# Kernel optimization log

Hardware: AMD Instinct MI355X
Metric: run time of the kernel (lower is better)

The kernel has to match this reference:

```python
import jax, jax.numpy as jnp
import numpy as np
from jax import lax

B = 64          # batch
IMG = 384       # image H=W
PATCH = 16      # stem patch size -> 24x24 grid
C = 192         # hidden_channels
K = 5           # knn_graph k (hard-coded in extract_graph)
HG = IMG // PATCH
N = HG * HG     # total_num_nodes = 576
HID = 4 * C     # FFN expansion
PRED_HID = 1024
NUM_CLASSES = 1


def setup_inputs() -> dict:
    key = jax.random.key(0)
    ks = jax.random.split(key, 16)
    def w(k, shape, s=0.02):
        return jax.random.normal(k, shape, jnp.float32) * s
    f32 = jnp.float32
    return {
        "x": jax.random.normal(ks[0], (B, 3, IMG, IMG), f32),
        # stem: 16x16 patch-embed conv
        "stem_w": w(ks[1], (C, 3, PATCH, PATCH)),
        "stem_b": jnp.zeros((C,), f32),
        "pos_embed": w(ks[2], (1, C, HG, HG)),
        # GSAT edge-attention MLP: concat(src,dst) -> C -> 1 -> sigmoid
        "att_w1": w(ks[3], (2 * C, C)), "att_b1": jnp.zeros((C,), f32),
        "att_w2": w(ks[4], (C, 1)),     "att_b2": jnp.zeros((1,), f32),
        # two message-passing layers (GIN-style update)
        "gnn_w1": w(ks[5], (C, C)), "gnn_b1": jnp.zeros((C,), f32),
        "gnn_w2": w(ks[6], (C, C)), "gnn_b2": jnp.zeros((C,), f32),
        # FFN (1x1 convs == channel matmuls), BN in eval mode (mean0/var1)
        "ffn_w1": w(ks[7], (C, HID)), "ffn_b1": jnp.zeros((HID,), f32),
        "ffn_g1": jnp.ones((HID,), f32), "ffn_be1": jnp.zeros((HID,), f32),
        "ffn_w2": w(ks[8], (HID, C)), "ffn_b2": jnp.zeros((C,), f32),
        "ffn_g2": jnp.ones((C,), f32), "ffn_be2": jnp.zeros((C,), f32),
        # prediction head: 1x1 conv C->1024, BN(eval), gelu, 1x1 conv 1024->num_classes
        "pred_w1": w(ks[9], (C, PRED_HID)), "pred_b1": jnp.zeros((PRED_HID,), f32),
        "pred_g": jnp.ones((PRED_HID,), f32), "pred_be": jnp.zeros((PRED_HID,), f32),
        "pred_w2": w(ks[10], (PRED_HID, NUM_CLASSES)), "pred_b2": jnp.zeros((NUM_CLASSES,), f32),
    }


def reference(x, stem_w, stem_b, pos_embed,
              att_w1, att_b1, att_w2, att_b2,
              gnn_w1, gnn_b1, gnn_w2, gnn_b2,
              ffn_w1, ffn_b1, ffn_g1, ffn_be1,
              ffn_w2, ffn_b2, ffn_g2, ffn_be2,
              pred_w1, pred_b1, pred_g, pred_be, pred_w2, pred_b2):
    # ---- stem + pos_embed ----
    feat = lax.conv_general_dilated(x, stem_w, (PATCH, PATCH), 'VALID',
                                    dimension_numbers=('NCHW', 'OIHW', 'NCHW'))
    feat = feat + stem_b[None, :, None, None] + pos_embed        # [B,C,Hg,Wg]
    b, c, hg, wg = feat.shape
    n = hg * wg
    nf = feat.reshape(b, c, n).transpose(0, 2, 1)                # [B,N,C]
    nfd = lax.stop_gradient(nf)                                  # extract_graph under no_grad

    # ---- kNN graph build: per-image pairwise sq. distances + top-k ----
    sq = jnp.sum(nfd * nfd, axis=-1)                             # [B,N]
    d2 = sq[:, :, None] + sq[:, None, :] - 2.0 * jnp.einsum('bnc,bmc->bnm', nfd, nfd)
    d2 = d2 + jnp.eye(n, dtype=d2.dtype) * 1e9                   # exclude self-loops
    _, idx = lax.top_k(-d2, K)                                   # [B,N,K] nearest neighbors
    src = (idx + (jnp.arange(b) * n)[:, None, None]).reshape(-1)  # [E] global neighbor idx
    dst = jnp.repeat(jnp.arange(b * n), K)                        # [E] global center idx

    # ---- GSAT GNN: edge attention + attention-weighted message passing ----
    h = nfd.reshape(b * n, c)                                    # [BN,C] (detached)
    e = jax.nn.relu(jnp.concatenate([h[src], h[dst]], axis=-1) @ att_w1 + att_b1)
    edge_att = jax.nn.sigmoid(e @ att_w2 + att_b2)               # [E,1]
    for Wg, bg in ((gnn_w1, gnn_b1), (gnn_w2, gnn_b2)):
        m = jax.ops.segment_sum(edge_att * h[src], dst, num_segments=b * n)
        h = jax.nn.relu((h + m) @ Wg + bg)                       # GIN-style update

    # ---- FFN (1x1 convs) with residual, BN eval-mode affine ----
    t = h.reshape(b, n, c)                                       # [B,N,C]
    u = jax.nn.gelu((t @ ffn_w1 + ffn_b1) * ffn_g1 + ffn_be1, approximate=False)
    t = t + ((u @ ffn_w2 + ffn_b2) * ffn_g2 + ffn_be2)

    # ---- global average pool + prediction head ----
    g = jnp.mean(t, axis=1)                                      # [B,C]
    p = jax.nn.gelu((g @ pred_w1 + pred_b1) * pred_g + pred_be, approximate=False)
    prediction = p @ pred_w2 + pred_b2                           # [B,num_classes]
    return edge_att, prediction
```

## Files before the change

### kernel.cpp

```cpp
#include <hip/hip_runtime.h>
#include <hip/hip_bf16.h>
#include <math.h>

constexpr int B_    = 64;
constexpr int C_    = 192;
constexpr int N_    = 576;
constexpr int BN_   = B_ * N_;
constexpr int K_    = 5;
constexpr int E_    = BN_ * K_;

__device__ __forceinline__ float gelu_exact(float x) {
    return 0.5f * x * (1.0f + erff(x * 0.70710678118654752440f));
}

__device__ __forceinline__ float bf2f(unsigned short v) {
    return __uint_as_float(((unsigned)v) << 16);
}
__device__ __forceinline__ unsigned short f2bf(float x) {
    __hip_bfloat16 h = __float2bfloat16(x);
    return *(unsigned short*)&h;
}

__global__ __launch_bounds__(256) void transpose_w_k(const float* __restrict__ w,
                                                     float* __restrict__ wt) {
    int gid = blockIdx.x * 256 + threadIdx.x;
    int k = gid / 192, oc = gid % 192;
    wt[gid] = w[oc * 768 + k];
}

__global__ __launch_bounds__(256) void stem_gemm96_k(
    const float* __restrict__ x, const float* __restrict__ Wt,
    const float* __restrict__ sb, const float* __restrict__ pos,
    float* __restrict__ nf)
{
    __shared__ float As[96][68];
    __shared__ float Ws[64][68];
    const int tid = threadIdx.x;
    const int tr = tid >> 4, tc = tid & 15;
    const int mb = blockIdx.x;
    const int nb = blockIdx.y;
    const int b  = mb / 6;
    const int n0 = (mb % 6) * 96;

    float4 acc[6];
    #pragma unroll
    for (int i = 0; i < 6; ++i) acc[i] = float4{0.f, 0.f, 0.f, 0.f};

    for (int kc = 0; kc < 768; kc += 64) {
        #pragma unroll
        for (int i = 0; i < 6; ++i) {
            int q = i * 256 + tid;
            int m = q >> 4, kq = q & 15;
            int k = kc + kq * 4;
            int ci = k >> 8, rem = k & 255, dy = rem >> 4, dx = rem & 15;
            int n = n0 + m, py = n / 24, px = n % 24;
            const float* src = &x[(((size_t)(b * 3 + ci) * 384) + py * 16 + dy) * 384
                                  + px * 16 + dx];
            *(float4*)&As[m][kq * 4] = *(const float4*)src;
        }
        #pragma unroll
        for (int i = 0; i < 4; ++i) {
            int q = i * 256 + tid;
            int m = q >> 4, kq = q & 15;
            *(float4*)&Ws[m][kq * 4] =
                *(const float4*)&Wt[(size_t)(kc + m) * 192 + nb * 64 + kq * 4];
        }
        __syncthreads();
        #pragma unroll
        for (int k4 = 0; k4 < 64; k4 += 4) {
            float4 a4[6], b4[4];
            #pragma unroll
            for (int i = 0; i < 6; ++i) a4[i] = *(const float4*)&As[tr * 6 + i][k4];
            #pragma unroll
            for (int kk = 0; kk < 4; ++kk) b4[kk] = *(const float4*)&Ws[k4 + kk][tc * 4];
            #pragma unroll
            for (int i = 0; i < 6; ++i) {
                const float av[4] = {a4[i].x, a4[i].y, a4[i].z, a4[i].w};
                #pragma unroll
                for (int kk = 0; kk < 4; ++kk) {
                    acc[i].x += av[kk] * b4[kk].x;
                    acc[i].y += av[kk] * b4[kk].y;
                    acc[i].z += av[kk] * b4[kk].z;
                    acc[i].w += av[kk] * b4[kk].w;
                }
            }
        }
        __syncthreads();
    }

    #pragma unroll
    for (int i = 0; i < 6; ++i) {
        int n = n0 + tr * 6 + i;
        int row = b * 576 + n;
        int oc0 = nb * 64 + tc * 4;
        float v[4] = {acc[i].x, acc[i].y, acc[i].z, acc[i].w};
        #pragma unroll
        for (int j = 0; j < 4; ++j) {
            int oc = oc0 + j;
            v[j] = v[j] + sb[oc] + pos[oc * 576 + n];
        }
        *(float4*)&nf[(size_t)row * 192 + oc0] = float4{v[0], v[1], v[2], v[3]};
    }
}

__global__ __launch_bounds__(256) void sq_k(const float* __restrict__ nf,
                                            float* __restrict__ sq) {
    int wid = threadIdx.x >> 6, lane = threadIdx.x & 63;
    int n = blockIdx.x * 4 + wid;
    const float* row = nf + (size_t)n * 192;
    float s = 0.f;
    #pragma unroll
    for (int c = 0; c < 3; ++c) { float v = row[lane + c * 64]; s += v * v; }
    #pragma unroll
    for (int off = 32; off; off >>= 1) s += __shfl_down(s, off);
    if (lane == 0) sq[n] = s;
}

__global__ void transpose_nf_k(const float* __restrict__ nf, float* __restrict__ nfT) {
    __shared__ float tile[32][33];
    int b = blockIdx.z;
    int n0 = blockIdx.x * 32, c0 = blockIdx.y * 32;
    int tx = threadIdx.x, ty = threadIdx.y;
    #pragma unroll
    for (int r = 0; r < 4; ++r) {
        int i = ty * 4 + r;
        tile[i][tx] = nf[((size_t)b * 576 + n0 + i) * 192 + c0 + tx];
    }
    __syncthreads();
    #pragma unroll
    for (int r = 0; r < 4; ++r) {
        int i = ty * 4 + r;
        nfT[((size_t)b * 192 + c0 + i) * 576 + n0 + tx] = tile[tx][i];
    }
}

__global__ __launch_bounds__(256) void knn_part_k(
    const float* __restrict__ nf, const float* __restrict__ nfT,
    const float* __restrict__ sqn, float* __restrict__ candV,
    int* __restrict__ candI)
{
    __shared__ float As[64][68];
    __shared__ float Cs[64][68];
    __shared__ float d2s[64][69];
    const int tid = threadIdx.x;
    const int tr = tid >> 4, tc = tid & 15;
    const int b = blockIdx.x;
    const int row0 = blockIdx.y * 64;
    const int gz = blockIdx.z;
    const int cc0 = gz * 3;

    float* mergeV = (float*)&As[0][0];
    int*   mergeI = (int*)&Cs[0][0];

    float tv[5];
    int ti[5];
    #pragma unroll
    for (int p = 0; p < 5; ++p) { tv[p] = 3.4e38f; ti[p] = 0; }

    for (int cc = cc0; cc < cc0 + 3; ++cc) {
        float4 acc[4];
        acc[0] = acc[1] = acc[2] = acc[3] = float4{0.f, 0.f, 0.f, 0.f};
        for (int kc = 0; kc < 192; kc += 64) {
            #pragma unroll
            for (int i = 0; i < 4; ++i) {
                int q = i * 256 + tid;
                int m = q >> 4, kq = q & 15;
                *(float4*)&As[m][kq * 4] =
                    *(const float4*)&nf[((size_t)(b * 576 + row0 + m)) * 192 + kc + kq * 4];
                *(float4*)&Cs[m][kq * 4] =
                    *(const float4*)&nfT[((size_t)(b * 192 + kc + m)) * 576 + cc * 64 + kq * 4];
            }
            __syncthreads();
            #pragma unroll
            for (int k4 = 0; k4 < 64; k4 += 4) {
                float4 a4[4], b4[4];
                #pragma unroll
                for (int i = 0; i < 4; ++i) a4[i] = *(const float4*)&As[tr * 4 + i][k4];
                #pragma unroll
                for (int kk = 0; kk < 4; ++kk) b4[kk] = *(const float4*)&Cs[k4 + kk][tc * 4];
                #pragma unroll
                for (int i = 0; i < 4; ++i) {
                    const float av[4] = {a4[i].x, a4[i].y, a4[i].z, a4[i].w};
                    #pragma unroll
                    for (int kk = 0; kk < 4; ++kk) {
                        acc[i].x += av[kk] * b4[kk].x;
                        acc[i].y += av[kk] * b4[kk].y;
                        acc[i].z += av[kk] * b4[kk].z;
                        acc[i].w += av[kk] * b4[kk].w;
                    }
                }
            }
            __syncthreads();
        }
        #pragma unroll
        for (int i = 0; i < 4; ++i) {
            int rl = tr * 4 + i, rg = row0 + rl;
            float sr = sqn[b * 576 + rg];
            float vv[4] = {acc[i].x, acc[i].y, acc[i].z, acc[i].w};
            #pragma unroll
            for (int j = 0; j < 4; ++j) {
                int cl = tc * 4 + j, cg = cc * 64 + cl;
                float d = sr + sqn[b * 576 + cg] - 2.f * vv[j];
                if (cg == rg) d += 1e9f;
                d2s[rl][cl] = d;
            }
        }
        __syncthreads();

        {
            const int r = tid & 63, p = tid >> 6;
            float pv[5]; int pi[5];
            #pragma unroll
            for (int q = 0; q < 5; ++q) { pv[q] = 3.4e38f; pi[q] = 0x7fffffff; }
            #pragma unroll
            for (int j = 0; j < 16; ++j) {
                int c = p * 16 + j;
                float cv = d2s[r][c];
                if (cv < pv[4]) {
                    int ci = cc * 64 + c;
                    #pragma unroll
                    for (int q = 0; q < 5; ++q) {
                        bool less = cv < pv[q];
                        float nv = less ? pv[q] : cv;
                        int ni   = less ? pi[q] : ci;
                        pv[q] = less ? cv : pv[q];
                        pi[q] = less ? ci : pi[q];
                        cv = nv; ci = ni;
                    }
                }
            }
            #pragma unroll
            for (int q = 0; q < 5; ++q) {
                mergeV[r * 21 + p * 5 + q] = pv[q];
                mergeI[r * 21 + p * 5 + q] = pi[q];
            }
        }
        __syncthreads();
        if (tid < 64) {
            for (int s = 0; s < 20; ++s) {
                float cv = mergeV[tid * 21 + s];
                if (cv < tv[4]) {
                    int cidx = mergeI[tid * 21 + s];
                    #pragma unroll
                    for (int q = 0; q < 5; ++q) {
                        bool less = cv < tv[q];
                        float nv = less ? tv[q] : cv;
                        int ni   = less ? ti[q] : cidx;
                        tv[q] = less ? cv : tv[q];
                        ti[q] = less ? cidx : ti[q];
                        cv = nv; cidx = ni;
                    }
                }
            }
        }
        __syncthreads();
    }
    if (tid < 64) {
        int gr = b * 576 + row0 + tid;
        #pragma unroll
        for (int p = 0; p < 5; ++p) {
            candV[(size_t)gr * 15 + gz * 5 + p] = tv[p];
            candI[(size_t)gr * 15 + gz * 5 + p] = ti[p];
        }
    }
}

__global__ __launch_bounds__(256) void knn_merge_k(
    const float* __restrict__ candV, const int* __restrict__ candI,
    int* __restrict__ idxOut)
{
    int r = blockIdx.x * 256 + threadIdx.x;
    float tv[5]; int ti[5];
    #pragma unroll
    for (int p = 0; p < 5; ++p) { tv[p] = 3.4e38f; ti[p] = 0; }
    #pragma unroll
    for (int s = 0; s < 15; ++s) {
        float cv = candV[(size_t)r * 15 + s];
        if (cv < tv[4]) {
            int cidx = candI[(size_t)r * 15 + s];
            #pragma unroll
            for (int q = 0; q < 5; ++q) {
                bool less = cv < tv[q];
                float nv = less ? tv[q] : cv;
                int ni   = less ? ti[q] : cidx;
                tv[q] = less ? cv : tv[q];
                ti[q] = less ? cidx : ti[q];
                cv = nv; cidx = ni;
            }
        }
    }
    int base = (r / 576) * 576;
    #pragma unroll
    for (int p = 0; p < 5; ++p) idxOut[r * 5 + p] = base + ti[p];
}

template <int EPI>
__global__ __launch_bounds__(256) void gemm_rm_k(
    const float* __restrict__ A, const float* __restrict__ W, float* __restrict__ out,
    int M, int N, int K,
    const float* __restrict__ bias, const float* __restrict__ gsc,
    const float* __restrict__ gsh, const float* __restrict__ res)
{
    __shared__ float As[64][68];
    __shared__ float Ws[64][68];
    const int tid = threadIdx.x;
    const int tr = tid >> 4, tc = tid & 15;
    const int mBase = blockIdx.x * 64, nBase = blockIdx.y * 64;

    float4 acc[4];
    acc[0] = acc[1] = acc[2] = acc[3] = float4{0.f, 0.f, 0.f, 0.f};

    for (int kc = 0; kc < K; kc += 64) {
        #pragma unroll
        for (int i = 0; i < 4; ++i) {
            int q = i * 256 + tid;
            int m = q >> 4, kq = q & 15;
            *(float4*)&As[m][kq * 4] =
                *(const float4*)&A[(size_t)(mBase + m) * K + kc + kq * 4];
            *(float4*)&Ws[m][kq * 4] =
                *(const float4*)&W[(size_t)(kc + m) * N + nBase + kq * 4];
        }
        __syncthreads();
        #pragma unroll
        for (int k4 = 0; k4 < 64; k4 += 4) {
            float4 a4[4], b4[4];
            #pragma unroll
            for (int i = 0; i < 4; ++i) a4[i] = *(const float4*)&As[tr * 4 + i][k4];
            #pragma unroll
            for (int kk = 0; kk < 4; ++kk) b4[kk] = *(const float4*)&Ws[k4 + kk][tc * 4];
            #pragma unroll
            for (int i = 0; i < 4; ++i) {
                const float av[4] = {a4[i].x, a4[i].y, a4[i].z, a4[i].w};
                #pragma unroll
                for (int kk = 0; kk < 4; ++kk) {
                    acc[i].x += av[kk] * b4[kk].x;
                    acc[i].y += av[kk] * b4[kk].y;
                    acc[i].z += av[kk] * b4[kk].z;
                    acc[i].w += av[kk] * b4[kk].w;
                }
            }
        }
        __syncthreads();
    }

    #pragma unroll
    for (int i = 0; i < 4; ++i) {
        int row = mBase + tr * 4 + i;
        int n0 = nBase + tc * 4;
        float v[4] = {acc[i].x, acc[i].y, acc[i].z, acc[i].w};
        #pragma unroll
        for (int j = 0; j < 4; ++j) {
            int n = n0 + j;
            float xv = v[j];
            if (EPI == 1) xv += bias[n];
            if (EPI == 2) { xv += bias[n]; xv = fmaxf(xv, 0.f); }
            if (EPI == 3) { xv = (xv + bias[n]) * gsc[n] + gsh[n]; xv = gelu_exact(xv); }
            if (EPI == 4) {
                xv = res[(size_t)row * N + n] + (xv + bias[n]) * gsc[n] + gsh[n];
            }
            v[j] = xv;
        }
        *(float4*)&out[(size_t)row * N + n0] = float4{v[0], v[1], v[2], v[3]};
    }
}

template <int EPI>
__global__ __launch_bounds__(256) void gemm_mfma_k(
    const unsigned short* __restrict__ A, const unsigned short* __restrict__ Bt,
    unsigned short* __restrict__ out, int M, int N, int K,
    const float* __restrict__ bias, const float* __restrict__ gsc,
    const float* __restrict__ gsh, const unsigned short* __restrict__ res)
{
    using frag = __attribute__((ext_vector_type(8))) short;
    using facc = __attribute__((ext_vector_type(4))) float;
    __shared__ unsigned short As[64][72];
    __shared__ unsigned short Bs[64][72];
    const int tid = threadIdx.x;
    const int wave = tid >> 6, lane = tid & 63;
    const int m16 = lane & 15, quad = lane >> 4;
    const int mBase = blockIdx.x * 64, nBase = blockIdx.y * 64;

    facc zero = {0.f, 0.f, 0.f, 0.f};
    facc acc[4];
    #pragma unroll
    for (int t = 0; t < 4; ++t) acc[t] = zero;

    for (int kc = 0; kc < K; kc += 64) {
        #pragma unroll
        for (int r = 0; r < 2; ++r) {
            int q = r * 256 + tid;
            int row = q >> 3, c8 = (q & 7) * 8;
            *(int4*)&As[row][c8] =
                *(const int4*)&A[(size_t)(mBase + row) * K + kc + c8];
            *(int4*)&Bs[row][c8] =
                *(const int4*)&Bt[(size_t)(nBase + row) * K + kc + c8];
        }
        __syncthreads();
        #pragma unroll
        for (int kk = 0; kk < 64; kk += 32) {
            frag a = *(const frag*)&As[16 * wave + m16][kk + quad * 8];
            #pragma unroll
            for (int t = 0; t < 4; ++t) {
                frag b = *(const frag*)&Bs[t * 16 + m16][kk + quad * 8];
                acc[t] = __builtin_amdgcn_mfma_f32_16x16x32_bf16(a, b, acc[t], 0, 0, 0);
            }
        }
        __syncthreads();
    }

    #pragma unroll
    for (int t = 0; t < 4; ++t) {
        #pragma unroll
        for (int r = 0; r < 4; ++r) {
            int row = mBase + 16 * wave + quad * 4 + r;
            int col = nBase + t * 16 + m16;
            float xv = acc[t][r];
            if (EPI == 2) { xv += bias[col]; xv = fmaxf(xv, 0.f); }
            if (EPI == 3) { xv = (xv + bias[col]) * gsc[col] + gsh[col]; xv = gelu_exact(xv); }
            if (EPI == 4) {
                xv = bf2f(res[(size_t)row * N + col]) + (xv + bias[col]) * gsc[col] + gsh[col];
            }
            out[(size_t)row * N + col] = f2bf(xv);
        }
    }
}

template <int EPI>
__global__ __launch_bounds__(256) void gemm_mfma_split_k(
    const unsigned short* __restrict__ Ah, const unsigned short* __restrict__ Al,
    const unsigned short* __restrict__ Bh, const unsigned short* __restrict__ Bl,
    float* __restrict__ out, int M, int N, int K, const float* __restrict__ bias)
{
    using frag = __attribute__((ext_vector_type(8))) short;
    using facc = __attribute__((ext_vector_type(4))) float;
    __shared__ unsigned short AsH[64][72], AsL[64][72];
    __shared__ unsigned short BsH[64][72], BsL[64][72];
    const int tid = threadIdx.x;
    const int wave = tid >> 6, lane = tid & 63;
    const int m16 = lane & 15, quad = lane >> 4;
    const int mBase = blockIdx.x * 64, nBase = blockIdx.y * 64;

    facc zero = {0.f, 0.f, 0.f, 0.f};
    facc acc[4];
    #pragma unroll
    for (int t = 0; t < 4; ++t) acc[t] = zero;

    for (int kc = 0; kc < K; kc += 64) {
        #pragma unroll
        for (int r = 0; r < 2; ++r) {
            int q = r * 256 + tid;
            int row = q >> 3, c8 = (q & 7) * 8;
            *(int4*)&AsH[row][c8] = *(const int4*)&Ah[(size_t)(mBase + row) * K + kc + c8];
            *(int4*)&AsL[row][c8] = *(const int4*)&Al[(size_t)(mBase + row) * K + kc + c8];
            *(int4*)&BsH[row][c8] = *(const int4*)&Bh[(size_t)(nBase + row) * K + kc + c8];
            *(int4*)&BsL[row][c8] = *(const int4*)&Bl[(size_t)(nBase + row) * K + kc + c8];
        }
        __syncthreads();
        #pragma unroll
        for (int kk = 0; kk < 64; kk += 32) {
            frag ah = *(const frag*)&AsH[16 * wave + m16][kk + quad * 8];
            frag al = *(const frag*)&AsL[16 * wave + m16][kk + quad * 8];
            #pragma unroll
            for (int t = 0; t < 4; ++t) {
                frag bh = *(const frag*)&BsH[t * 16 + m16][kk + quad * 8];
                frag bl = *(const frag*)&BsL[t * 16 + m16][kk + quad * 8];
                acc[t] = __builtin_amdgcn_mfma_f32_16x16x32_bf16(ah, bh, acc[t], 0, 0, 0);
                acc[t] = __builtin_amdgcn_mfma_f32_16x16x32_bf16(ah, bl, acc[t], 0, 0, 0);
                acc[t] = __builtin_amdgcn_mfma_f32_16x16x32_bf16(al, bh, acc[t], 0, 0, 0);
            }
        }
        __syncthreads();
    }

    #pragma unroll
    for (int t = 0; t < 4; ++t) {
        #pragma unroll
        for (int r = 0; r < 4; ++r) {
            int row = mBase + 16 * wave + quad * 4 + r;
            int col = nBase + t * 16 + m16;
            float xv = acc[t][r];
            if (EPI == 1) xv += bias[col];
            out[(size_t)row * N + col] = xv;
        }
    }
}

__global__ __launch_bounds__(256) void asplit_k(const float* __restrict__ a,
                                                unsigned short* __restrict__ hi,
                                                unsigned short* __restrict__ lo) {
    int g = blockIdx.x * 256 + threadIdx.x;
    float v = a[g];
    unsigned short h = f2bf(v);
    hi[g] = h;
    lo[g] = f2bf(v - bf2f(h));
}

__global__ __launch_bounds__(256) void wsplit_att_k(const float* __restrict__ w,
                                                    unsigned short* __restrict__ hi,
                                                    unsigned short* __restrict__ lo) {
    int gid = blockIdx.x * 256 + threadIdx.x;
    int half = gid / 36864, r = gid % 36864;
    int n = r / 192, k = r % 192;
    float v = w[(size_t)(half * 192 + k) * 192 + n];
    unsigned short h = f2bf(v);
    hi[gid] = h;
    lo[gid] = f2bf(v - bf2f(h));
}

__global__ __launch_bounds__(256) void wprep_k(const float* __restrict__ w,
                                               unsigned short* __restrict__ wt,
                                               int K, int N) {
    int gid = blockIdx.x * 256 + threadIdx.x;
    int n = gid / K, k = gid % K;
    wt[gid] = f2bf(w[(size_t)k * N + n]);
}

__global__ __launch_bounds__(256) void edge_att_k(
    const float* __restrict__ hA, const float* __restrict__ hB,
    const int* __restrict__ idx, const float* __restrict__ w2,
    const float* __restrict__ b2, float* __restrict__ att)
{
    int wid = threadIdx.x >> 6, lane = threadIdx.x & 63;
    int e = blockIdx.x * 4 + wid;
    int dst = e / K_;
    int src = idx[e];
    float s = 0.f;
    #pragma unroll
    for (int c0 = 0; c0 < 3; ++c0) {
        int c = lane + c0 * 64;
        float v = hA[(size_t)src * 192 + c] + hB[(size_t)dst * 192 + c];
        v = fmaxf(v, 0.f);
        s += v * w2[c];
    }
    #pragma unroll
    for (int off = 32; off; off >>= 1) s += __shfl_down(s, off);
    if (lane == 0) att[e] = 1.f / (1.f + expf(-(s + b2[0])));
}

__device__ __forceinline__ float ldv(const float* p, size_t i) { return p[i]; }
__device__ __forceinline__ float ldv(const unsigned short* p, size_t i) { return bf2f(p[i]); }

template <typename TI>
__global__ __launch_bounds__(256) void msg_bf_k(
    const TI* __restrict__ h, const float* __restrict__ att,
    const int* __restrict__ idx, unsigned short* __restrict__ s)
{
    int g = blockIdx.x * 256 + threadIdx.x;
    int n = g / 192, c = g % 192;
    float acc = ldv(h, (size_t)g);
    #pragma unroll
    for (int p = 0; p < K_; ++p) {
        int sp = idx[n * K_ + p];
        acc += att[n * K_ + p] * ldv(h, (size_t)sp * 192 + c);
    }
    s[g] = f2bf(acc);
}

__global__ void pool_bf16_k(const unsigned short* __restrict__ t, float* __restrict__ g) {
    int b = blockIdx.x, c = threadIdx.x;
    float s = 0.f;
    for (int n = 0; n < 576; ++n) s += bf2f(t[((size_t)b * 576 + n) * 192 + c]);
    g[b * 192 + c] = s * (1.f / 576.f);
}

__global__ __launch_bounds__(256) void head2_k(
    const float* __restrict__ p, const float* __restrict__ w2,
    const float* __restrict__ b2, float* __restrict__ out)
{
    int b = blockIdx.x;
    float s = 0.f;
    for (int j = threadIdx.x; j < 1024; j += 256) s += p[(size_t)b * 1024 + j] * w2[j];
    #pragma unroll
    for (int off = 32; off; off >>= 1) s += __shfl_down(s, off);
    __shared__ float ls[4];
    int wid = threadIdx.x >> 6, lane = threadIdx.x & 63;
    if (lane == 0) ls[wid] = s;
    __syncthreads();
    if (threadIdx.x == 0) out[b] = ls[0] + ls[1] + ls[2] + ls[3] + b2[0];
}

extern "C" void kernel_launch(void* const* d_in, const int* in_sizes, int n_in,
                              void* d_out, int out_size, void* d_ws, size_t ws_size,
                              hipStream_t stream) {
    const float* x        = (const float*)d_in[0];
    const float* stem_w   = (const float*)d_in[1];
    const float* stem_b   = (const float*)d_in[2];
    const float* pos      = (const float*)d_in[3];
    const float* att_w1   = (const float*)d_in[4];
    const float* att_b1   = (const float*)d_in[5];
    const float* att_w2   = (const float*)d_in[6];
    const float* att_b2   = (const float*)d_in[7];
    const float* gnn_w1   = (const float*)d_in[8];
    const float* gnn_b1   = (const float*)d_in[9];
    const float* gnn_w2   = (const float*)d_in[10];
    const float* gnn_b2   = (const float*)d_in[11];
    const float* ffn_w1   = (const float*)d_in[12];
    const float* ffn_b1   = (const float*)d_in[13];
    const float* ffn_g1   = (const float*)d_in[14];
    const float* ffn_be1  = (const float*)d_in[15];
    const float* ffn_w2   = (const float*)d_in[16];
    const float* ffn_b2   = (const float*)d_in[17];
    const float* ffn_g2   = (const float*)d_in[18];
    const float* ffn_be2  = (const float*)d_in[19];
    const float* pred_w1  = (const float*)d_in[20];
    const float* pred_b1  = (const float*)d_in[21];
    const float* pred_g   = (const float*)d_in[22];
    const float* pred_be  = (const float*)d_in[23];
    const float* pred_w2  = (const float*)d_in[24];
    const float* pred_b2  = (const float*)d_in[25];

    float* ws = (float*)d_ws;
    const size_t RSZ = (size_t)BN_ * C_;
    float* R0 = ws;
    float* R1 = R0 + RSZ;
    float* R2 = R1 + RSZ;
    float* R3 = R2 + RSZ;
    float* sqb = R3 + RSZ;
    int*   idxb = (int*)(sqb + BN_);
    float* gb = (float*)(idxb + E_);
    float* pb = gb + 64 * C_;
    unsigned short* wg1T = (unsigned short*)(pb + 64 * 1024);
    unsigned short* wg2T = wg1T + 192 * 192;
    unsigned short* wf1T = wg2T + 192 * 192;
    unsigned short* wf2T = wf1T + 768 * 192;
    unsigned short* waHi = wf2T + 192 * 768;
    unsigned short* waLo = waHi + 2 * 192 * 192;
    float* candV = (float*)(waLo + 2 * 192 * 192);
    int*   candI = (int*)(candV + (size_t)BN_ * 15);

    unsigned short* Sb    = (unsigned short*)R1;
    unsigned short* Hb    = (unsigned short*)(R1 + RSZ / 2);
    unsigned short* Tb    = (unsigned short*)R2;
    unsigned short* ToutB = (unsigned short*)(R2 + RSZ / 2);
    unsigned short* Ahi   = (unsigned short*)R3;
    unsigned short* Alo   = Ahi + RSZ;
    unsigned short* Ub    = (unsigned short*)R3;

    float* att  = (float*)d_out;
    float* pred = att + E_;

    float* Wt = R3;

    wprep_k<<<144, 256, 0, stream>>>(gnn_w1, wg1T, 192, 192);
    wprep_k<<<144, 256, 0, stream>>>(gnn_w2, wg2T, 192, 192);
    wprep_k<<<576, 256, 0, stream>>>(ffn_w1, wf1T, 192, 768);
    wprep_k<<<576, 256, 0, stream>>>(ffn_w2, wf2T, 768, 192);
    wsplit_att_k<<<288, 256, 0, stream>>>(att_w1, waHi, waLo);

    transpose_w_k<<<576, 256, 0, stream>>>(stem_w, Wt);
    stem_gemm96_k<<<dim3(384, 3), 256, 0, stream>>>(x, Wt, stem_b, pos, R0);

    sq_k<<<BN_ / 4, 256, 0, stream>>>(R0, sqb);
    transpose_nf_k<<<dim3(18, 6, 64), dim3(32, 8), 0, stream>>>(R0, R3);
    knn_part_k<<<dim3(64, 9, 3), 256, 0, stream>>>(R0, R3, sqb, candV, candI);
    knn_merge_k<<<BN_ / 256, 256, 0, stream>>>(candV, candI, idxb);

    asplit_k<<<BN_ * C_ / 256, 256, 0, stream>>>(R0, Ahi, Alo);
    gemm_mfma_split_k<0><<<dim3(576, 3), 256, 0, stream>>>(Ahi, Alo,
        waHi, waLo, R1, BN_, 192, 192, nullptr);
    gemm_mfma_split_k<1><<<dim3(576, 3), 256, 0, stream>>>(Ahi, Alo,
        waHi + 36864, waLo + 36864, R2, BN_, 192, 192, att_b1);
    edge_att_k<<<E_ / 4, 256, 0, stream>>>(R1, R2, idxb, att_w2, att_b2, att);

    msg_bf_k<float><<<BN_ * C_ / 256, 256, 0, stream>>>(R0, att, idxb, Sb);
    gemm_mfma_k<2><<<dim3(576, 3), 256, 0, stream>>>(Sb, wg1T, Hb,
        BN_, 192, 192, gnn_b1, nullptr, nullptr, nullptr);
    msg_bf_k<unsigned short><<<BN_ * C_ / 256, 256, 0, stream>>>(Hb, att, idxb, Sb);
    gemm_mfma_k<2><<<dim3(576, 3), 256, 0, stream>>>(Sb, wg2T, Tb,
        BN_, 192, 192, gnn_b2, nullptr, nullptr, nullptr);

    for (int ch = 0; ch < 2; ++ch) {
        const unsigned short* Ain = Tb + (size_t)ch * 18432 * 192;
        unsigned short* Tout = ToutB + (size_t)ch * 18432 * 192;
        gemm_mfma_k<3><<<dim3(288, 12), 256, 0, stream>>>(Ain, wf1T, Ub,
            18432, 768, 192, ffn_b1, ffn_g1, ffn_be1, nullptr);
        gemm_mfma_k<4><<<dim3(288, 3), 256, 0, stream>>>(Ub, wf2T, Tout,
            18432, 192, 768, ffn_b2, ffn_g2, ffn_be2, Ain);
    }

    pool_bf16_k<<<64, 192, 0, stream>>>(ToutB, gb);
    gemm_rm_k<3><<<dim3(1, 16), 256, 0, stream>>>(gb, pred_w1, pb,
        64, 1024, 192, pred_b1, pred_g, pred_be, nullptr);
    head2_k<<<64, 256, 0, stream>>>(pb, pred_w2, pred_b2, pred);
}
```

Measured before the change: 808.2 us.

## Exploit distance symmetry in kNN: compute upper-triangle tiles once, emit both directions

Replaces the kNN partial kernel with one that computes only the 45 upper-triangular 64x64 tiles of each per-image distance matrix. Each tile produces top-5 candidates for its rows and, for off-diagonal tiles, also for its columns, so roughly half the distance GEMM work is removed. Blocks shrink to 64 threads with an 8x8 register tile, both operands are read from the transposed features, and candidate buffers are reused from an existing workspace region. The merge kernel now scans 45 candidates per row instead of 15. Smaller blocks and the serial 64-element scans per thread may lower occupancy and parallelism.

```diff
diff --git a/kernel.cpp b/kernel.cpp
--- a/kernel.cpp
+++ b/kernel.cpp
@@ -134,133 +134,124 @@
     }
 }
 
-__global__ __launch_bounds__(256) void knn_part_k(
-    const float* __restrict__ nf, const float* __restrict__ nfT,
-    const float* __restrict__ sqn, float* __restrict__ candV,
-    int* __restrict__ candI)
-{
-    __shared__ float As[64][68];
-    __shared__ float Cs[64][68];
-    __shared__ float d2s[64][69];
+__global__ __launch_bounds__(64) void knn_sym_k(
+    const float* __restrict__ nfT, const float* __restrict__ sqn,
+    float* __restrict__ candV, int* __restrict__ candI)
+{
+    __shared__ float smem[64 * 69];
+    float* As  = smem;
+    float* Bs  = smem + 2048;
+    float* d2s = smem;
+
     const int tid = threadIdx.x;
-    const int tr = tid >> 4, tc = tid & 15;
-    const int b = blockIdx.x;
-    const int row0 = blockIdx.y * 64;
-    const int gz = blockIdx.z;
-    const int cc0 = gz * 3;
-
-    float* mergeV = (float*)&As[0][0];
-    int*   mergeI = (int*)&Cs[0][0];
-
-    float tv[5];
-    int ti[5];
-    #pragma unroll
-    for (int p = 0; p < 5; ++p) { tv[p] = 3.4e38f; ti[p] = 0; }
-
-    for (int cc = cc0; cc < cc0 + 3; ++cc) {
-        float4 acc[4];
-        acc[0] = acc[1] = acc[2] = acc[3] = float4{0.f, 0.f, 0.f, 0.f};
-        for (int kc = 0; kc < 192; kc += 64) {
-            #pragma unroll
-            for (int i = 0; i < 4; ++i) {
-                int q = i * 256 + tid;
-                int m = q >> 4, kq = q & 15;
-                *(float4*)&As[m][kq * 4] =
-                    *(const float4*)&nf[((size_t)(b * 576 + row0 + m)) * 192 + kc + kq * 4];
-                *(float4*)&Cs[m][kq * 4] =
-                    *(const float4*)&nfT[((size_t)(b * 192 + kc + m)) * 576 + cc * 64 + kq * 4];
-            }
-            __syncthreads();
-            #pragma unroll
-            for (int k4 = 0; k4 < 64; k4 += 4) {
-                float4 a4[4], b4[4];
+    const int tr = tid >> 3, tc = tid & 7;
+    const int b = blockIdx.y;
+    int t = blockIdx.x;
+    int bi = 0;
+    while (t >= 9 - bi) { t -= 9 - bi; ++bi; }
+    const int bj = bi + t;
+    const int r0 = bi * 64, c0 = bj * 64;
+
+    float acc[8][8];
+    #pragma unroll
+    for (int i = 0; i < 8; ++i)
+        #pragma unroll
+        for (int j = 0; j < 8; ++j) acc[i][j] = 0.f;
+
+    for (int kc = 0; kc < 192; kc += 32) {
+        #pragma unroll
+        for (int i = 0; i < 8; ++i) {
+            int q = i * 64 + tid;
+            int k = q >> 4, c4 = (q & 15) * 4;
+            const float* srow = &nfT[((size_t)(b * 192 + kc + k)) * 576];
+            *(float4*)&As[k * 64 + c4] = *(const float4*)&srow[r0 + c4];
+            *(float4*)&Bs[k * 64 + c4] = *(const float4*)&srow[c0 + c4];
+        }
+        __syncthreads();
+        #pragma unroll 8
+        for (int kk = 0; kk < 32; ++kk) {
+            float4 a0 = *(const float4*)&As[kk * 64 + tr * 8];
+            float4 a1 = *(const float4*)&As[kk * 64 + tr * 8 + 4];
+            float4 b0 = *(const float4*)&Bs[kk * 64 + tc * 8];
+            float4 b1 = *(const float4*)&Bs[kk * 64 + tc * 8 + 4];
+            const float av[8] = {a0.x, a0.y, a0.z, a0.w, a1.x, a1.y, a1.z, a1.w};
+            const float bv[8] = {b0.x, b0.y, b0.z, b0.w, b1.x, b1.y, b1.z, b1.w};
+            #pragma unroll
+            for (int i = 0; i < 8; ++i)
                 #pragma unroll
-                for (int i = 0; i < 4; ++i) a4[i] = *(const float4*)&As[tr * 4 + i][k4];
+                for (int j = 0; j < 8; ++j)
+                    acc[i][j] += av[i] * bv[j];
+        }
+        __syncthreads();
+    }
+
+    #pragma unroll
+    for (int i = 0; i < 8; ++i) {
+        int rl = tr * 8 + i, rg = r0 + rl;
+        float sr = sqn[b * 576 + rg];
+        #pragma unroll
+        for (int j = 0; j < 8; ++j) {
+            int cl = tc * 8 + j, cg = c0 + cl;
+            float d = sr + sqn[b * 576 + cg] - 2.f * acc[i][j];
+            if (cg == rg) d += 1e9f;
+            d2s[rl * 69 + cl] = d;
+        }
+    }
+    __syncthreads();
+
+    {
+        const int r = tid;
+        float tv[5]; int ti[5];
+        #pragma unroll
+        for (int p = 0; p < 5; ++p) { tv[p] = 3.4e38f; ti[p] = 0; }
+        for (int c = 0; c < 64; ++c) {
+            float cv = d2s[r * 69 + c];
+            if (cv < tv[4]) {
+                int ci = c0 + c;
                 #pragma unroll
-                for (int kk = 0; kk < 4; ++kk) b4[kk] = *(const float4*)&Cs[k4 + kk][tc * 4];
+                for (int q = 0; q < 5; ++q) {
+                    bool less = cv < tv[q];
+                    float nv = less ? tv[q] : cv;
+                    int ni   = less ? ti[q] : ci;
+                    tv[q] = less ? cv : tv[q];
+                    ti[q] = less ? ci : ti[q];
+                    cv = nv; ci = ni;
+                }
+            }
+        }
+        int gr = b * 576 + r0 + r;
+        #pragma unroll
+        for (int p = 0; p < 5; ++p) {
+            candV[(size_t)gr * 45 + bj * 5 + p] = tv[p];
+            candI[(size_t)gr * 45 + bj * 5 + p] = ti[p];
+        }
+    }
+
+    if (bi != bj) {
+        const int c = tid;
+        float tv[5]; int ti[5];
+        #pragma unroll
+        for (int p = 0; p < 5; ++p) { tv[p] = 3.4e38f; ti[p] = 0; }
+        for (int r = 0; r < 64; ++r) {
+            float cv = d2s[r * 69 + c];
+            if (cv < tv[4]) {
+                int ci = r0 + r;
                 #pragma unroll
-                for (int i = 0; i < 4; ++i) {
-                    const float av[4] = {a4[i].x, a4[i].y, a4[i].z, a4[i].w};
-                    #pragma unroll
-                    for (int kk = 0; kk < 4; ++kk) {
-                        acc[i].x += av[kk] * b4[kk].x;
-                        acc[i].y += av[kk] * b4[kk].y;
-                        acc[i].z += av[kk] * b4[kk].z;
-                        acc[i].w += av[kk] * b4[kk].w;
-                    }
+                for (int q = 0; q < 5; ++q) {
+                    bool less = cv < tv[q];
+                    float nv = less ? tv[q] : cv;
+                    int ni   = less ? ti[q] : ci;
+                    tv[q] = less ? cv : tv[q];
+                    ti[q] = less ? ci : ti[q];
+                    cv = nv; ci = ni;
                 }
             }
-            __syncthreads();
-        }
-        #pragma unroll
-        for (int i = 0; i < 4; ++i) {
-            int rl = tr * 4 + i, rg = row0 + rl;
-            float sr = sqn[b * 576 + rg];
-            float vv[4] = {acc[i].x, acc[i].y, acc[i].z, acc[i].w};
-            #pragma unroll
-            for (int j = 0; j < 4; ++j) {
-                int cl = tc * 4 + j, cg = cc * 64 + cl;
-                float d = sr + sqn[b * 576 + cg] - 2.f * vv[j];
-                if (cg == rg) d += 1e9f;
-                d2s[rl][cl] = d;
-            }
-        }
-        __syncthreads();
-
-        {
-            const int r = tid & 63, p = tid >> 6;
-            float pv[5]; int pi[5];
-            #pragma unroll
-            for (int q = 0; q < 5; ++q) { pv[q] = 3.4e38f; pi[q] = 0x7fffffff; }
-            #pragma unroll
-            for (int j = 0; j < 16; ++j) {
-                int c = p * 16 + j;
-                float cv = d2s[r][c];
-                if (cv < pv[4]) {
-                    int ci = cc * 64 + c;
-                    #pragma unroll
-                    for (int q = 0; q < 5; ++q) {
-                        bool less = cv < pv[q];
-                        float nv = less ? pv[q] : cv;
-                        int ni   = less ? pi[q] : ci;
-                        pv[q] = less ? cv : pv[q];
-                        pi[q] = less ? ci : pi[q];
-                        cv = nv; ci = ni;
-                    }
-                }
-            }
-            #pragma unroll
-            for (int q = 0; q < 5; ++q) {
-                mergeV[r * 21 + p * 5 + q] = pv[q];
-                mergeI[r * 21 + p * 5 + q] = pi[q];
-            }
-        }
-        __syncthreads();
-        if (tid < 64) {
-            for (int s = 0; s < 20; ++s) {
-                float cv = mergeV[tid * 21 + s];
-                if (cv < tv[4]) {
-                    int cidx = mergeI[tid * 21 + s];
-                    #pragma unroll
-                    for (int q = 0; q < 5; ++q) {
-                        bool less = cv < tv[q];
-                        float nv = less ? tv[q] : cv;
-                        int ni   = less ? ti[q] : cidx;
-                        tv[q] = less ? cv : tv[q];
-                        ti[q] = less ? cidx : ti[q];
-                        cv = nv; cidx = ni;
-                    }
-                }
-            }
-        }
-        __syncthreads();
-    }
-    if (tid < 64) {
-        int gr = b * 576 + row0 + tid;
+        }
+        int gr = b * 576 + c0 + c;
         #pragma unroll
         for (int p = 0; p < 5; ++p) {
-            candV[(size_t)gr * 15 + gz * 5 + p] = tv[p];
-            candI[(size_t)gr * 15 + gz * 5 + p] = ti[p];
+            candV[(size_t)gr * 45 + bi * 5 + p] = tv[p];
+            candI[(size_t)gr * 45 + bi * 5 + p] = ti[p];
         }
     }
 }
@@ -273,11 +264,11 @@
     float tv[5]; int ti[5];
     #pragma unroll
     for (int p = 0; p < 5; ++p) { tv[p] = 3.4e38f; ti[p] = 0; }
-    #pragma unroll
-    for (int s = 0; s < 15; ++s) {
-        float cv = candV[(size_t)r * 15 + s];
+    #pragma unroll 5
+    for (int s = 0; s < 45; ++s) {
+        float cv = candV[(size_t)r * 45 + s];
         if (cv < tv[4]) {
-            int cidx = candI[(size_t)r * 15 + s];
+            int cidx = candI[(size_t)r * 45 + s];
             #pragma unroll
             for (int q = 0; q < 5; ++q) {
                 bool less = cv < tv[q];
@@ -625,8 +616,9 @@
     unsigned short* wf2T = wf1T + 768 * 192;
     unsigned short* waHi = wf2T + 192 * 768;
     unsigned short* waLo = waHi + 2 * 192 * 192;
-    float* candV = (float*)(waLo + 2 * 192 * 192);
-    int*   candI = (int*)(candV + (size_t)BN_ * 15);
+
+    float* candV = R1;
+    int*   candI = (int*)(R1 + (size_t)BN_ * 45);
 
     unsigned short* Sb    = (unsigned short*)R1;
     unsigned short* Hb    = (unsigned short*)(R1 + RSZ / 2);
@@ -652,7 +644,7 @@
 
     sq_k<<<BN_ / 4, 256, 0, stream>>>(R0, sqb);
     transpose_nf_k<<<dim3(18, 6, 64), dim3(32, 8), 0, stream>>>(R0, R3);
-    knn_part_k<<<dim3(64, 9, 3), 256, 0, stream>>>(R0, R3, sqb, candV, candI);
+    knn_sym_k<<<dim3(45, 64), 64, 0, stream>>>(R3, sqb, candV, candI);
     knn_merge_k<<<BN_ / 256, 256, 0, stream>>>(candV, candI, idxb);
 
     asplit_k<<<BN_ * C_ / 256, 256, 0, stream>>>(R0, Ahi, Alo);
```

After: 780.7 us. -3.4%, faster.

## Exploit distance-matrix symmetry in kNN by computing only upper-triangular tiles

Applied to the files above, without the earlier changes.

Replaces the row-block kNN kernel with one that computes only the 45 upper-triangular 64x64 tile pairs per batch and derives top-5 candidates for both the row block and the column block from each off-diagonal tile. This roughly halves the pairwise distance GEMM work. In exchange the merge kernel must scan 45 candidates per row instead of 15. The candidate buffers move into reused workspace R1.

```diff
diff --git a/kernel.cpp b/kernel.cpp
--- a/kernel.cpp
+++ b/kernel.cpp
@@ -134,133 +134,188 @@
     }
 }
 
-__global__ __launch_bounds__(256) void knn_part_k(
+__global__ __launch_bounds__(256) void knn_sym2_k(
     const float* __restrict__ nf, const float* __restrict__ nfT,
     const float* __restrict__ sqn, float* __restrict__ candV,
     int* __restrict__ candI)
 {
-    __shared__ float As[64][68];
-    __shared__ float Cs[64][68];
-    __shared__ float d2s[64][69];
+    __shared__ float smem[9792];
+    float (*As)[68]  = (float(*)[68])smem;
+    float (*Cs)[68]  = (float(*)[68])(smem + 4352);
+    float (*d2s)[69] = (float(*)[69])smem;
+    float* mAV = smem + 4416;
+    int*   mAI = (int*)(smem + 5760);
+    float* mBV = smem + 7104;
+    int*   mBI = (int*)(smem + 8448);
+
     const int tid = threadIdx.x;
     const int tr = tid >> 4, tc = tid & 15;
-    const int b = blockIdx.x;
-    const int row0 = blockIdx.y * 64;
-    const int gz = blockIdx.z;
-    const int cc0 = gz * 3;
-
-    float* mergeV = (float*)&As[0][0];
-    int*   mergeI = (int*)&Cs[0][0];
-
-    float tv[5];
-    int ti[5];
-    #pragma unroll
-    for (int p = 0; p < 5; ++p) { tv[p] = 3.4e38f; ti[p] = 0; }
-
-    for (int cc = cc0; cc < cc0 + 3; ++cc) {
-        float4 acc[4];
-        acc[0] = acc[1] = acc[2] = acc[3] = float4{0.f, 0.f, 0.f, 0.f};
-        for (int kc = 0; kc < 192; kc += 64) {
+    const int b = blockIdx.y;
+    int t = blockIdx.x;
+    int bi = 0;
+    while (t >= 9 - bi) { t -= 9 - bi; ++bi; }
+    const int bj = bi + t;
+    const int row0 = bi * 64, c0 = bj * 64;
+
+    float4 acc[4];
+    acc[0] = acc[1] = acc[2] = acc[3] = float4{0.f, 0.f, 0.f, 0.f};
+    for (int kc = 0; kc < 192; kc += 64) {
+        #pragma unroll
+        for (int i = 0; i < 4; ++i) {
+            int q = i * 256 + tid;
+            int m = q >> 4, kq = q & 15;
+            *(float4*)&As[m][kq * 4] =
+                *(const float4*)&nf[((size_t)(b * 576 + row0 + m)) * 192 + kc + kq * 4];
+            *(float4*)&Cs[m][kq * 4] =
+                *(const float4*)&nfT[((size_t)(b * 192 + kc + m)) * 576 + c0 + kq * 4];
+        }
+        __syncthreads();
+        #pragma unroll
+        for (int k4 = 0; k4 < 64; k4 += 4) {
+            float4 a4[4], b4[4];
+            #pragma unroll
+            for (int i = 0; i < 4; ++i) a4[i] = *(const float4*)&As[tr * 4 + i][k4];
+            #pragma unroll
+            for (int kk = 0; kk < 4; ++kk) b4[kk] = *(const float4*)&Cs[k4 + kk][tc * 4];
             #pragma unroll
             for (int i = 0; i < 4; ++i) {
-                int q = i * 256 + tid;
-                int m = q >> 4, kq = q & 15;
-                *(float4*)&As[m][kq * 4] =
-                    *(const float4*)&nf[((size_t)(b * 576 + row0 + m)) * 192 + kc + kq * 4];
-                *(float4*)&Cs[m][kq * 4] =
-                    *(const float4*)&nfT[((size_t)(b * 192 + kc + m)) * 576 + cc * 64 + kq * 4];
-            }
-            __syncthreads();
-            #pragma unroll
-            for (int k4 = 0; k4 < 64; k4 += 4) {
-                float4 a4[4], b4[4];
+                const float av[4] = {a4[i].x, a4[i].y, a4[i].z, a4[i].w};
                 #pragma unroll
-                for (int i = 0; i < 4; ++i) a4[i] = *(const float4*)&As[tr * 4 + i][k4];
+                for (int kk = 0; kk < 4; ++kk) {
+                    acc[i].x += av[kk] * b4[kk].x;
+                    acc[i].y += av[kk] * b4[kk].y;
+                    acc[i].z += av[kk] * b4[kk].z;
+                    acc[i].w += av[kk] * b4[kk].w;
+                }
+            }
+        }
+        __syncthreads();
+    }
+
+    #pragma unroll
+    for (int i = 0; i < 4; ++i) {
+        int rl = tr * 4 + i, rg = row0 + rl;
+        float sr = sqn[b * 576 + rg];
+        float vv[4] = {acc[i].x, acc[i].y, acc[i].z, acc[i].w};
+        #pragma unroll
+        for (int j = 0; j < 4; ++j) {
+            int cl = tc * 4 + j, cg = c0 + cl;
+            float d = sr + sqn[b * 576 + cg] - 2.f * vv[j];
+            if (cg == rg) d += 1e9f;
+            d2s[rl][cl] = d;
+        }
+    }
+    __syncthreads();
+
+    {
+        const int r = tid & 63, p = tid >> 6;
+        float pv[5]; int pi[5];
+        #pragma unroll
+        for (int q = 0; q < 5; ++q) { pv[q] = 3.4e38f; pi[q] = 0x7fffffff; }
+        #pragma unroll
+        for (int j = 0; j < 16; ++j) {
+            int c = p * 16 + j;
+            float cv = d2s[r][c];
+            if (cv < pv[4]) {
+                int ci = c0 + c;
                 #pragma unroll
-                for (int kk = 0; kk < 4; ++kk) b4[kk] = *(const float4*)&Cs[k4 + kk][tc * 4];
+                for (int q = 0; q < 5; ++q) {
+                    bool less = cv < pv[q];
+                    float nv = less ? pv[q] : cv;
+                    int ni   = less ? pi[q] : ci;
+                    pv[q] = less ? cv : pv[q];
+                    pi[q] = less ? ci : pi[q];
+                    cv = nv; ci = ni;
+                }
+            }
+        }
+        #pragma unroll
+        for (int q = 0; q < 5; ++q) {
+            mAV[r * 21 + p * 5 + q] = pv[q];
+            mAI[r * 21 + p * 5 + q] = pi[q];
+        }
+    }
+
+    if (bi != bj) {
+        const int c = tid & 63, p = tid >> 6;
+        float pv[5]; int pi[5];
+        #pragma unroll
+        for (int q = 0; q < 5; ++q) { pv[q] = 3.4e38f; pi[q] = 0x7fffffff; }
+        #pragma unroll
+        for (int j = 0; j < 16; ++j) {
+            int rr = p * 16 + j;
+            float cv = d2s[rr][c];
+            if (cv < pv[4]) {
+                int ci = row0 + rr;
                 #pragma unroll
-                for (int i = 0; i < 4; ++i) {
-                    const float av[4] = {a4[i].x, a4[i].y, a4[i].z, a4[i].w};
-                    #pragma unroll
-                    for (int kk = 0; kk < 4; ++kk) {
-                        acc[i].x += av[kk] * b4[kk].x;
-                        acc[i].y += av[kk] * b4[kk].y;
-                        acc[i].z += av[kk] * b4[kk].z;
-                        acc[i].w += av[kk] * b4[kk].w;
-                    }
+                for (int q = 0; q < 5; ++q) {
+                    bool less = cv < pv[q];
+                    float nv = less ? pv[q] : cv;
+                    int ni   = less ? pi[q] : ci;
+                    pv[q] = less ? cv : pv[q];
+                    pi[q] = less ? ci : pi[q];
+                    cv = nv; ci = ni;
                 }
             }
-            __syncthreads();
-        }
-        #pragma unroll
-        for (int i = 0; i < 4; ++i) {
-            int rl = tr * 4 + i, rg = row0 + rl;
-            float sr = sqn[b * 576 + rg];
-            float vv[4] = {acc[i].x, acc[i].y, acc[i].z, acc[i].w};
-            #pragma unroll
-            for (int j = 0; j < 4; ++j) {
-                int cl = tc * 4 + j, cg = cc * 64 + cl;
-                float d = sr + sqn[b * 576 + cg] - 2.f * vv[j];
-                if (cg == rg) d += 1e9f;
-                d2s[rl][cl] = d;
-            }
-        }
-        __syncthreads();
-
-        {
-            const int r = tid & 63, p = tid >> 6;
-            float pv[5]; int pi[5];
-            #pragma unroll
-            for (int q = 0; q < 5; ++q) { pv[q] = 3.4e38f; pi[q] = 0x7fffffff; }
-            #pragma unroll
-            for (int j = 0; j < 16; ++j) {
-                int c = p * 16 + j;
-                float cv = d2s[r][c];
-                if (cv < pv[4]) {
-                    int ci = cc * 64 + c;
-                    #pragma unroll
-                    for (int q = 0; q < 5; ++q) {
-                        bool less = cv < pv[q];
-                        float nv = less ? pv[q] : cv;
-                        int ni   = less ? pi[q] : ci;
-                        pv[q] = less ? cv : pv[q];
-                        pi[q] = less ? ci : pi[q];
-                        cv = nv; ci = ni;
-                    }
+        }
+        #pragma unroll
+        for (int q = 0; q < 5; ++q) {
+            mBV[c * 21 + p * 5 + q] = pv[q];
+            mBI[c * 21 + p * 5 + q] = pi[q];
+        }
+    }
+    __syncthreads();
+
+    if (tid < 64) {
+        float tv[5]; int ti[5];
+        #pragma unroll
+        for (int p = 0; p < 5; ++p) { tv[p] = 3.4e38f; ti[p] = 0; }
+        for (int s = 0; s < 20; ++s) {
+            float cv = mAV[tid * 21 + s];
+            if (cv < tv[4]) {
+                int cidx = mAI[tid * 21 + s];
+                #pragma unroll
+                for (int q = 0; q < 5; ++q) {
+                    bool less = cv < tv[q];
+                    float nv = less ? tv[q] : cv;
+                    int ni   = less ? ti[q] : cidx;
+                    tv[q] = less ? cv : tv[q];
+                    ti[q] = less ? cidx : ti[q];
+                    cv = nv; cidx = ni;
                 }
             }
-            #pragma unroll
-            for (int q = 0; q < 5; ++q) {
-                mergeV[r * 21 + p * 5 + q] = pv[q];
-                mergeI[r * 21 + p * 5 + q] = pi[q];
-            }
-        }
-        __syncthreads();
-        if (tid < 64) {
-            for (int s = 0; s < 20; ++s) {
-                float cv = mergeV[tid * 21 + s];
-                if (cv < tv[4]) {
-                    int cidx = mergeI[tid * 21 + s];
-                    #pragma unroll
-                    for (int q = 0; q < 5; ++q) {
-                        bool less = cv < tv[q];
-                        float nv = less ? tv[q] : cv;
-                        int ni   = less ? ti[q] : cidx;
-                        tv[q] = less ? cv : tv[q];
-                        ti[q] = less ? cidx : ti[q];
-                        cv = nv; cidx = ni;
-                    }
+        }
+        int gr = b * 576 + row0 + tid;
+        #pragma unroll
+        for (int p = 0; p < 5; ++p) {
+            candV[(size_t)gr * 45 + bj * 5 + p] = tv[p];
+            candI[(size_t)gr * 45 + bj * 5 + p] = ti[p];
+        }
+    } else if (tid < 128 && bi != bj) {
+        int c = tid - 64;
+        float tv[5]; int ti[5];
+        #pragma unroll
+        for (int p = 0; p < 5; ++p) { tv[p] = 3.4e38f; ti[p] = 0; }
+        for (int s = 0; s < 20; ++s) {
+            float cv = mBV[c * 21 + s];
+            if (cv < tv[4]) {
+                int cidx = mBI[c * 21 + s];
+                #pragma unroll
+                for (int q = 0; q < 5; ++q) {
+                    bool less = cv < tv[q];
+                    float nv = less ? tv[q] : cv;
+                    int ni   = less ? ti[q] : cidx;
+                    tv[q] = less ? cv : tv[q];
+                    ti[q] = less ? cidx : ti[q];
+                    cv = nv; cidx = ni;
                 }
             }
         }
-        __syncthreads();
-    }
-    if (tid < 64) {
-        int gr = b * 576 + row0 + tid;
+        int gr = b * 576 + c0 + c;
         #pragma unroll
         for (int p = 0; p < 5; ++p) {
-            candV[(size_t)gr * 15 + gz * 5 + p] = tv[p];
-            candI[(size_t)gr * 15 + gz * 5 + p] = ti[p];
+            candV[(size_t)gr * 45 + bi * 5 + p] = tv[p];
+            candI[(size_t)gr * 45 + bi * 5 + p] = ti[p];
         }
     }
 }
@@ -273,11 +328,11 @@
     float tv[5]; int ti[5];
     #pragma unroll
     for (int p = 0; p < 5; ++p) { tv[p] = 3.4e38f; ti[p] = 0; }
-    #pragma unroll
-    for (int s = 0; s < 15; ++s) {
-        float cv = candV[(size_t)r * 15 + s];
+    #pragma unroll 5
+    for (int s = 0; s < 45; ++s) {
+        float cv = candV[(size_t)r * 45 + s];
         if (cv < tv[4]) {
-            int cidx = candI[(size_t)r * 15 + s];
+            int cidx = candI[(size_t)r * 45 + s];
             #pragma unroll
             for (int q = 0; q < 5; ++q) {
                 bool less = cv < tv[q];
@@ -625,8 +680,9 @@
     unsigned short* wf2T = wf1T + 768 * 192;
     unsigned short* waHi = wf2T + 192 * 768;
     unsigned short* waLo = waHi + 2 * 192 * 192;
-    float* candV = (float*)(waLo + 2 * 192 * 192);
-    int*   candI = (int*)(candV + (size_t)BN_ * 15);
+
+    float* candV = R1;
+    int*   candI = (int*)(R1 + (size_t)BN_ * 45);
 
     unsigned short* Sb    = (unsigned short*)R1;
     unsigned short* Hb    = (unsigned short*)(R1 + RSZ / 2);
@@ -652,7 +708,7 @@
 
     sq_k<<<BN_ / 4, 256, 0, stream>>>(R0, sqb);
     transpose_nf_k<<<dim3(18, 6, 64), dim3(32, 8), 0, stream>>>(R0, R3);
-    knn_part_k<<<dim3(64, 9, 3), 256, 0, stream>>>(R0, R3, sqb, candV, candI);
+    knn_sym2_k<<<dim3(45, 64), 256, 0, stream>>>(R0, R3, sqb, candV, candI);
     knn_merge_k<<<BN_ / 256, 256, 0, stream>>>(candV, candI, idxb);
 
     asplit_k<<<BN_ * C_ / 256, 256, 0, stream>>>(R0, Ahi, Alo);
```

After: 800.2 us. No clear change (-1.0%).
